# Kernel tuning notes

Measured on AMD Instinct MI355X. Metric: run time of the kernel, lower is better.

## Reference

```python
import jax, jax.numpy as jnp
import numpy as np

B, S, D, H = 4, 1024, 1024, 16
DK = D // H
EPS_LN = 1e-6

def setup_inputs() -> dict:
    key = jax.random.key(0)
    ks = jax.random.split(key, 16)
    sc = 1.0 / np.sqrt(D)
    inp = {}
    names = ['q_r','q_i','k_r','k_i','v_r','v_i']
    for i, n in enumerate(names):
        inp[n] = jax.random.normal(ks[i], (B, S, D), dtype=jnp.float32)
    wnames = ['wq_r','wq_i','wk_r','wk_i','wv_r','wv_i','wfc_r','wfc_i']
    for i, n in enumerate(wnames):
        inp[n] = jax.random.normal(ks[6 + i], (D, D), dtype=jnp.float32) * sc
    inp['gamma'] = jnp.ones((D,), dtype=jnp.float32)
    inp['beta'] = jnp.zeros((D,), dtype=jnp.float32)
    return inp

def _clinear(xr, xi, wr, wi):
    # complex (xr + i*xi) @ (wr + i*wi)^T, weights stored [out, in]
    r = xr @ wr.T - xi @ wi.T
    im = xi @ wr.T + xr @ wi.T
    return r, im

def _forward(q_r, q_i, k_r, k_i, v_r, v_i, wq_r, wq_i, wk_r, wk_i,
             wv_r, wv_i, wfc_r, wfc_i, gamma, beta):
    res_r, res_i = q_r, q_i
    qr, qi = _clinear(q_r, q_i, wq_r, wq_i)
    kr, ki = _clinear(k_r, k_i, wk_r, wk_i)
    vr, vi = _clinear(v_r, v_i, wv_r, wv_i)
    # [B,S,D] -> [B,H,S,DK]
    split = lambda x: x.reshape(B, S, H, DK).transpose(0, 2, 1, 3)
    qr, qi, kr, ki, vr, vi = map(split, (qr, qi, kr, ki, vr, vi))
    temp = jnp.asarray(DK ** 0.5, qr.dtype)
    qr = qr / temp
    qi = qi / temp
    # q @ conj(k)^T : real = qr.kr + qi.ki ; imag = qi.kr - qr.ki
    ar = jnp.einsum('bhqd,bhkd->bhqk', qr, kr) + jnp.einsum('bhqd,bhkd->bhqk', qi, ki)
    ai = jnp.einsum('bhqd,bhkd->bhqk', qi, kr) - jnp.einsum('bhqd,bhkd->bhqk', qr, ki)
    attn = jax.nn.softmax(jnp.sqrt(ar * ar + ai * ai), axis=-1)  # magnitude softmax
    or_ = jnp.einsum('bhqk,bhkd->bhqd', attn, vr)
    oi_ = jnp.einsum('bhqk,bhkd->bhqd', attn, vi)
    merge = lambda x: x.transpose(0, 2, 1, 3).reshape(B, S, D)
    or_, oi_ = merge(or_), merge(oi_)
    fr, fi = _clinear(or_, oi_, wfc_r, wfc_i)
    # ComplexDropout in eval mode: identity except imag += 1e-10
    fi = fi + 1e-10
    xr = fr + res_r
    xi = fi + res_i
    # ComplexLayerNorm: mean over all non-batch dims, elementwise magnitude norm
    mr = jnp.mean(xr, axis=(1, 2), keepdims=True)
    mi = jnp.mean(xi, axis=(1, 2), keepdims=True)
    cr = xr - mr
    ci = xi - mi
    std = jnp.sqrt(cr * cr + ci * ci + EPS_LN)
    yr = gamma * (cr / std) + beta
    yi = gamma * (ci / std)
    return yr, yi, attn

def reference(q_r, q_i, k_r, k_i, v_r, v_i, wq_r, wq_i, wk_r, wk_i,
              wv_r, wv_i, wfc_r, wfc_i, gamma, beta):
    return _forward(q_r, q_i, k_r, k_i, v_r, v_i, wq_r, wq_i, wk_r, wk_i,
                    wv_r, wv_i, wfc_r, wfc_i, gamma, beta)
```

## Files before the change

### kernel.cpp

```cpp
#include <hip/hip_runtime.h>
#include <math.h>

#define NB 4
#define SEQ 1024
#define DIM 1024
#define NH 16
#define DHEAD 64
#define BUFN 4194304ULL
#define WHN  1048576ULL
#define LOG2E 1.4426950408889634f

typedef _Float16 f16x8 __attribute__((ext_vector_type(8)));
typedef _Float16 f16x4 __attribute__((ext_vector_type(4)));
typedef float    f32x4 __attribute__((ext_vector_type(4)));

#define MFMA16 __builtin_amdgcn_mfma_f32_16x16x32_f16

__device__ __forceinline__ void split4(const float4 v, f16x4& h, f16x4& l)
{
    const _Float16 h0=(_Float16)v.x, h1=(_Float16)v.y, h2=(_Float16)v.z, h3=(_Float16)v.w;
    h = (f16x4){h0, h1, h2, h3};
    l = (f16x4){(_Float16)((v.x-(float)h0)*2048.0f),
                (_Float16)((v.y-(float)h1)*2048.0f),
                (_Float16)((v.z-(float)h2)*2048.0f),
                (_Float16)((v.w-(float)h3)*2048.0f)};
}

__global__ __launch_bounds__(256)
void splitx_kernel(const float* __restrict__ xr, const float* __restrict__ xi,
                   _Float16* __restrict__ XS)
{
    const float* x = blockIdx.y ? xi : xr;
    _Float16* h = XS + (size_t)blockIdx.y * 2 * BUFN;
    _Float16* l = h + BUFN;
    const int i = (blockIdx.x * 256 + threadIdx.x) << 2;
    const float4 v = *(const float4*)(x + i);
    f16x4 hh, ll; split4(v, hh, ll);
    *(f16x4*)(h + i) = hh;
    *(f16x4*)(l + i) = ll;
}

__global__ __launch_bounds__(256)
void splitw_kernel(const float* w0, const float* w1, const float* w2, const float* w3,
                   const float* w4, const float* w5, const float* w6, const float* w7,
                   _Float16* __restrict__ WS)
{
    const int y = blockIdx.y;
    const float* x = (y==0)?w0:(y==1)?w1:(y==2)?w2:(y==3)?w3:(y==4)?w4:(y==5)?w5:(y==6)?w6:w7;
    _Float16* h = WS + (size_t)y * 2 * WHN;
    _Float16* l = h + WHN;
    const int i = (blockIdx.x * 256 + threadIdx.x) << 2;
    float4 v = *(const float4*)(x + i);
    v.x *= 64.0f; v.y *= 64.0f; v.z *= 64.0f; v.w *= 64.0f;
    f16x4 hh, ll; split4(v, hh, ll);
    *(f16x4*)(h + i) = hh;
    *(f16x4*)(l + i) = ll;
}

template<int MODE>
__global__ __launch_bounds__(256, 1)
void cgemm16_kernel(const _Float16* __restrict__ Ahr, const _Float16* __restrict__ Alr,
                    const _Float16* __restrict__ Ahi, const _Float16* __restrict__ Ali,
                    const _Float16* __restrict__ Bhr, const _Float16* __restrict__ Blr,
                    const _Float16* __restrict__ Bhi, const _Float16* __restrict__ Bli,
                    float* __restrict__ outr, float* __restrict__ outi,
                    const float* __restrict__ resr, const float* __restrict__ resi,
                    float* __restrict__ msum, float scale)
{
    __shared__ __align__(16) _Float16 As[4][64][40];
    __shared__ __align__(16) _Float16 Bs[4][64][40];
    const int t    = threadIdx.x;
    const int lane = t & 63;
    const int w    = t >> 6;
    const int wm   = w >> 1, wn = w & 1;
    const int lr   = lane & 15;
    const int kc   = (lane >> 4) << 3;
    const int m0   = blockIdx.x * 64;
    const int o0   = blockIdx.y * 64;
    const int srow = t >> 2;
    const int sc8  = (t & 3) << 3;

    const size_t aoff = (size_t)(m0 + srow) * DIM + sc8;
    const size_t boff = (size_t)(o0 + srow) * DIM + sc8;

    f32x4 acc[2][2][4];
    #pragma unroll
    for (int i = 0; i < 2; ++i)
        #pragma unroll
        for (int j = 0; j < 2; ++j)
            #pragma unroll
            for (int c = 0; c < 4; ++c)
                acc[i][j][c] = (f32x4){0.f, 0.f, 0.f, 0.f};

    for (int k0 = 0; k0 < DIM; k0 += 32) {
        const uint4 va0 = *(const uint4*)(Ahr + aoff + k0);
        const uint4 va1 = *(const uint4*)(Alr + aoff + k0);
        const uint4 va2 = *(const uint4*)(Ahi + aoff + k0);
        const uint4 va3 = *(const uint4*)(Ali + aoff + k0);
        const uint4 vb0 = *(const uint4*)(Bhr + boff + k0);
        const uint4 vb1 = *(const uint4*)(Blr + boff + k0);
        const uint4 vb2 = *(const uint4*)(Bhi + boff + k0);
        const uint4 vb3 = *(const uint4*)(Bli + boff + k0);
        __syncthreads();
        *(uint4*)&As[0][srow][sc8] = va0;
        *(uint4*)&As[1][srow][sc8] = va1;
        *(uint4*)&As[2][srow][sc8] = va2;
        *(uint4*)&As[3][srow][sc8] = va3;
        *(uint4*)&Bs[0][srow][sc8] = vb0;
        *(uint4*)&Bs[1][srow][sc8] = vb1;
        *(uint4*)&Bs[2][srow][sc8] = vb2;
        *(uint4*)&Bs[3][srow][sc8] = vb3;
        __syncthreads();

        f16x8 a0[2], a1[2], a2[2], a3[2];
        #pragma unroll
        for (int mt = 0; mt < 2; ++mt) {
            const int ar = wm * 32 + mt * 16 + lr;
            a0[mt] = *(const f16x8*)&As[0][ar][kc];
            a1[mt] = *(const f16x8*)&As[1][ar][kc];
            a2[mt] = *(const f16x8*)&As[2][ar][kc];
            a3[mt] = *(const f16x8*)&As[3][ar][kc];
        }
        #pragma unroll
        for (int nt = 0; nt < 2; ++nt) {
            const int br = wn * 32 + nt * 16 + lr;
            const f16x8 bhr = *(const f16x8*)&Bs[0][br][kc];
            const f16x8 blr = *(const f16x8*)&Bs[1][br][kc];
            const f16x8 bhi = *(const f16x8*)&Bs[2][br][kc];
            const f16x8 bli = *(const f16x8*)&Bs[3][br][kc];
            const f16x8 bhiN = -bhi;
            const f16x8 bliN = -bli;
            #pragma unroll
            for (int mt = 0; mt < 2; ++mt) {
                acc[mt][nt][0] = MFMA16(a0[mt], bhr,  acc[mt][nt][0], 0, 0, 0);
                acc[mt][nt][0] = MFMA16(a2[mt], bhiN, acc[mt][nt][0], 0, 0, 0);
                acc[mt][nt][1] = MFMA16(a0[mt], blr,  acc[mt][nt][1], 0, 0, 0);
                acc[mt][nt][1] = MFMA16(a1[mt], bhr,  acc[mt][nt][1], 0, 0, 0);
                acc[mt][nt][1] = MFMA16(a2[mt], bliN, acc[mt][nt][1], 0, 0, 0);
                acc[mt][nt][1] = MFMA16(a3[mt], bhiN, acc[mt][nt][1], 0, 0, 0);
                acc[mt][nt][2] = MFMA16(a2[mt], bhr,  acc[mt][nt][2], 0, 0, 0);
                acc[mt][nt][2] = MFMA16(a0[mt], bhi,  acc[mt][nt][2], 0, 0, 0);
                acc[mt][nt][3] = MFMA16(a2[mt], blr,  acc[mt][nt][3], 0, 0, 0);
                acc[mt][nt][3] = MFMA16(a3[mt], bhr,  acc[mt][nt][3], 0, 0, 0);
                acc[mt][nt][3] = MFMA16(a0[mt], bli,  acc[mt][nt][3], 0, 0, 0);
                acc[mt][nt][3] = MFMA16(a1[mt], bhi,  acc[mt][nt][3], 0, 0, 0);
            }
        }
    }

    const float INVL = 1.0f / 2048.0f;
    if (MODE == 0) {
        #pragma unroll
        for (int mt = 0; mt < 2; ++mt)
            #pragma unroll
            for (int nt = 0; nt < 2; ++nt)
                #pragma unroll
                for (int r = 0; r < 4; ++r) {
                    const int mrow = m0 + wm * 32 + mt * 16 + ((lane >> 4)) * 4 + r;
                    const int ncol = o0 + wn * 32 + nt * 16 + lr;
                    const float cr = (acc[mt][nt][0][r] + acc[mt][nt][1][r] * INVL) * scale;
                    const float ci = (acc[mt][nt][2][r] + acc[mt][nt][3][r] * INVL) * scale;
                    const int b = mrow >> 10, s = mrow & 1023, h = ncol >> 6, dk = ncol & 63;
                    const size_t idx = (((size_t)b * NH + h) * SEQ + s) * DHEAD + dk;
                    outr[idx] = cr;
                    outi[idx] = ci;
                }
    } else {
        float sr = 0.f, si = 0.f;
        #pragma unroll
        for (int mt = 0; mt < 2; ++mt)
            #pragma unroll
            for (int nt = 0; nt < 2; ++nt)
                #pragma unroll
                for (int r = 0; r < 4; ++r) {
                    const int mrow = m0 + wm * 32 + mt * 16 + ((lane >> 4)) * 4 + r;
                    const int ncol = o0 + wn * 32 + nt * 16 + lr;
                    const size_t idx = (size_t)mrow * DIM + ncol;
                    const float cr = (acc[mt][nt][0][r] + acc[mt][nt][1][r] * INVL) * scale
                                     + resr[idx];
                    const float ci = (acc[mt][nt][2][r] + acc[mt][nt][3][r] * INVL) * scale
                                     + 1e-10f + resi[idx];
                    outr[idx] = cr;
                    outi[idx] = ci;
                    sr += cr; si += ci;
                }
        #pragma unroll
        for (int off = 32; off > 0; off >>= 1) { sr += __shfl_xor(sr, off); si += __shfl_xor(si, off); }
        __shared__ float wsum[8];
        if ((t & 63) == 0) { wsum[w * 2 + 0] = sr; wsum[w * 2 + 1] = si; }
        __syncthreads();
        if (t == 0) {
            atomicAdd(&msum[2 * (m0 >> 10) + 0], wsum[0] + wsum[2] + wsum[4] + wsum[6]);
            atomicAdd(&msum[2 * (m0 >> 10) + 1], wsum[1] + wsum[3] + wsum[5] + wsum[7]);
        }
    }
}

__global__ __launch_bounds__(256)
void vtrans_kernel(const float* __restrict__ VR, const float* __restrict__ VI,
                   _Float16* __restrict__ Trh, _Float16* __restrict__ Trl,
                   _Float16* __restrict__ Tih, _Float16* __restrict__ Til)
{
    __shared__ float sr[64][68];
    __shared__ float si[64][68];
    const int t = threadIdx.x;
    const int kb = blockIdx.x, bh = blockIdx.y;
    const size_t ibase = (size_t)bh * SEQ * DHEAD + (size_t)kb * 64 * DHEAD;
    const int row = t >> 4, c0 = (t & 15) << 2;
    #pragma unroll
    for (int it = 0; it < 4; ++it) {
        const float4 a = *(const float4*)(VR + ibase + (size_t)(row + 16*it) * DHEAD + c0);
        const float4 b = *(const float4*)(VI + ibase + (size_t)(row + 16*it) * DHEAD + c0);
        *(float4*)&sr[row + 16*it][c0] = a;
        *(float4*)&si[row + 16*it][c0] = b;
    }
    __syncthreads();
    const int dk = t >> 2, k0 = (t & 3) << 4;
    f16x8 hr[2], lr8[2], hi8[2], li8[2];
    #pragma unroll
    for (int kk = 0; kk < 16; ++kk) {
        const float xr = sr[k0 + kk][dk];
        const float xi = si[k0 + kk][dk];
        const _Float16 hxr = (_Float16)xr;
        const _Float16 hxi = (_Float16)xi;
        hr[kk>>3][kk&7]  = hxr;
        lr8[kk>>3][kk&7] = (_Float16)((xr - (float)hxr) * 2048.0f);
        hi8[kk>>3][kk&7] = hxi;
        li8[kk>>3][kk&7] = (_Float16)((xi - (float)hxi) * 2048.0f);
    }
    const size_t ob = ((size_t)bh * 64 + dk) * SEQ + kb * 64 + k0;
    *(f16x8*)(Trh + ob) = hr[0];  *(f16x8*)(Trh + ob + 8) = hr[1];
    *(f16x8*)(Trl + ob) = lr8[0]; *(f16x8*)(Trl + ob + 8) = lr8[1];
    *(f16x8*)(Tih + ob) = hi8[0]; *(f16x8*)(Tih + ob + 8) = hi8[1];
    *(f16x8*)(Til + ob) = li8[0]; *(f16x8*)(Til + ob + 8) = li8[1];
}

__global__ __launch_bounds__(256, 1)
void attn_scores_kernel(const float* __restrict__ QR, const float* __restrict__ QI,
                        const float* __restrict__ KR, const float* __restrict__ KI,
                        float* __restrict__ attn, float* __restrict__ Lbuf)
{
    __shared__ __align__(16) _Float16 Ks[4][64][72];
    __shared__ float red[2][64];
    const int t = threadIdx.x;
    const int lane = t & 63;
    const int w = t >> 6, wm = w >> 1, wn = w & 1;
    const int lr = lane & 15, g = lane >> 4, kc = g << 3;
    const int q0 = blockIdx.x * 64;
    const int bh = blockIdx.y;
    const size_t base = (size_t)bh * SEQ * DHEAD;
    const int srow = t >> 2, sc0 = (t & 3) << 4;

    #pragma unroll
    for (int c = 0; c < 4; ++c) {
        const float4 a = *(const float4*)(QR + base + (size_t)(q0 + srow) * DHEAD + sc0 + 4*c);
        const float4 b = *(const float4*)(QI + base + (size_t)(q0 + srow) * DHEAD + sc0 + 4*c);
        f16x4 h, l;
        split4(a, h, l);
        *(f16x4*)&Ks[0][srow][sc0 + 4*c] = h;
        *(f16x4*)&Ks[1][srow][sc0 + 4*c] = l;
        split4(b, h, l);
        *(f16x4*)&Ks[2][srow][sc0 + 4*c] = h;
        *(f16x4*)&Ks[3][srow][sc0 + 4*c] = l;
    }
    __syncthreads();
    f16x8 qhr[2][2], qlr[2][2], qhi[2][2], qli[2][2];
    #pragma unroll
    for (int mt = 0; mt < 2; ++mt) {
        const int row = wm * 32 + mt * 16 + lr;
        #pragma unroll
        for (int ks = 0; ks < 2; ++ks) {
            const int col = ks * 32 + kc;
            qhr[mt][ks] = *(const f16x8*)&Ks[0][row][col];
            qlr[mt][ks] = *(const f16x8*)&Ks[1][row][col];
            qhi[mt][ks] = *(const f16x8*)&Ks[2][row][col];
            qli[mt][ks] = *(const f16x8*)&Ks[3][row][col];
        }
    }

    float lsum[2][4] = {};
    float4 pr[4], pi4[4];
    #pragma unroll
    for (int c = 0; c < 4; ++c) {
        pr[c]  = *(const float4*)(KR + base + (size_t)srow * DHEAD + sc0 + 4*c);
        pi4[c] = *(const float4*)(KI + base + (size_t)srow * DHEAD + sc0 + 4*c);
    }

    for (int kt = 0; kt < 16; ++kt) {
        __syncthreads();
        #pragma unroll
        for (int c = 0; c < 4; ++c) {
            f16x4 h, l;
            split4(pr[c], h, l);
            *(f16x4*)&Ks[0][srow][sc0 + 4*c] = h;
            *(f16x4*)&Ks[1][srow][sc0 + 4*c] = l;
            split4(pi4[c], h, l);
            *(f16x4*)&Ks[2][srow][sc0 + 4*c] = h;
            *(f16x4*)&Ks[3][srow][sc0 + 4*c] = l;
        }
        __syncthreads();
        if (kt < 15) {
            const size_t koff = base + (size_t)((kt + 1) * 64 + srow) * DHEAD;
            #pragma unroll
            for (int c = 0; c < 4; ++c) {
                pr[c]  = *(const float4*)(KR + koff + sc0 + 4*c);
                pi4[c] = *(const float4*)(KI + koff + sc0 + 4*c);
            }
        }
        f32x4 arh[2][2], arl[2][2], aih[2][2], ail[2][2];
        #pragma unroll
        for (int i = 0; i < 2; ++i)
            #pragma unroll
            for (int j = 0; j < 2; ++j) {
                arh[i][j] = (f32x4){0,0,0,0}; arl[i][j] = (f32x4){0,0,0,0};
                aih[i][j] = (f32x4){0,0,0,0}; ail[i][j] = (f32x4){0,0,0,0};
            }
        #pragma unroll
        for (int nt = 0; nt < 2; ++nt) {
            const int brow = wn * 32 + nt * 16 + lr;
            #pragma unroll
            for (int ks = 0; ks < 2; ++ks) {
                const int col = ks * 32 + kc;
                const f16x8 khr = *(const f16x8*)&Ks[0][brow][col];
                const f16x8 klr = *(const f16x8*)&Ks[1][brow][col];
                const f16x8 khi = *(const f16x8*)&Ks[2][brow][col];
                const f16x8 kli = *(const f16x8*)&Ks[3][brow][col];
                const f16x8 khiN = -khi;
                const f16x8 kliN = -kli;
                #pragma unroll
                for (int mt = 0; mt < 2; ++mt) {
                    arh[mt][nt] = MFMA16(qhr[mt][ks], khr,  arh[mt][nt], 0,0,0);
                    arh[mt][nt] = MFMA16(qhi[mt][ks], khi,  arh[mt][nt], 0,0,0);
                    arl[mt][nt] = MFMA16(qhr[mt][ks], klr,  arl[mt][nt], 0,0,0);
                    arl[mt][nt] = MFMA16(qlr[mt][ks], khr,  arl[mt][nt], 0,0,0);
                    arl[mt][nt] = MFMA16(qhi[mt][ks], kli,  arl[mt][nt], 0,0,0);
                    arl[mt][nt] = MFMA16(qli[mt][ks], khi,  arl[mt][nt], 0,0,0);
                    aih[mt][nt] = MFMA16(qhi[mt][ks], khr,  aih[mt][nt], 0,0,0);
                    aih[mt][nt] = MFMA16(qhr[mt][ks], khiN, aih[mt][nt], 0,0,0);
                    ail[mt][nt] = MFMA16(qhi[mt][ks], klr,  ail[mt][nt], 0,0,0);
                    ail[mt][nt] = MFMA16(qli[mt][ks], khr,  ail[mt][nt], 0,0,0);
                    ail[mt][nt] = MFMA16(qhr[mt][ks], kliN, ail[mt][nt], 0,0,0);
                    ail[mt][nt] = MFMA16(qlr[mt][ks], khiN, ail[mt][nt], 0,0,0);
                }
            }
        }
        const float INV = 1.0f / 2048.0f;
        #pragma unroll
        for (int mt = 0; mt < 2; ++mt)
            #pragma unroll
            for (int nt = 0; nt < 2; ++nt)
                #pragma unroll
                for (int r = 0; r < 4; ++r) {
                    const float ar = arh[mt][nt][r] + arl[mt][nt][r] * INV;
                    const float ai = aih[mt][nt][r] + ail[mt][nt][r] * INV;
                    const float s  = sqrtf(ar * ar + ai * ai);
                    const int q = q0 + wm * 32 + mt * 16 + g * 4 + r;
                    const int k = kt * 64 + wn * 32 + nt * 16 + lr;
                    attn[((size_t)bh * SEQ + q) * SEQ + k] = s;
                    lsum[mt][r] += exp2f(s * LOG2E);
                }
    }
    #pragma unroll
    for (int mt = 0; mt < 2; ++mt)
        #pragma unroll
        for (int r = 0; r < 4; ++r) {
            float v = lsum[mt][r];
            v += __shfl_xor(v, 1); v += __shfl_xor(v, 2);
            v += __shfl_xor(v, 4); v += __shfl_xor(v, 8);
            lsum[mt][r] = v;
        }
    if (lr == 0) {
        #pragma unroll
        for (int mt = 0; mt < 2; ++mt)
            #pragma unroll
            for (int r = 0; r < 4; ++r)
                red[wn][wm * 32 + mt * 16 + g * 4 + r] = lsum[mt][r];
    }
    __syncthreads();
    if (t < 64) Lbuf[(size_t)bh * SEQ + q0 + t] = red[0][t] + red[1][t];
}

__global__ __launch_bounds__(256, 1)
void attn_pv_kernel(float* __restrict__ attn, const float* __restrict__ Lbuf,
                    const _Float16* __restrict__ Trh, const _Float16* __restrict__ Trl,
                    const _Float16* __restrict__ Tih, const _Float16* __restrict__ Til,
                    _Float16* __restrict__ XOhr, _Float16* __restrict__ XOlr,
                    _Float16* __restrict__ XOhi, _Float16* __restrict__ XOli)
{
    __shared__ __align__(16) _Float16 Ps[2][64][72];
    __shared__ float invL[64];
    const int t = threadIdx.x;
    const int lane = t & 63;
    const int w = t >> 6, wm = w >> 1, wn = w & 1;
    const int lr = lane & 15, g = lane >> 4, kc = g << 3;
    const int q0 = blockIdx.x * 64;
    const int bh = blockIdx.y;
    const size_t abase = ((size_t)bh * SEQ + q0) * SEQ;
    const size_t vbase = (size_t)bh * 64 * SEQ;

    if (t < 64) invL[t] = 1.0f / Lbuf[(size_t)bh * SEQ + q0 + t];

    const size_t vrow[2] = { vbase + (size_t)(wn * 32 + lr) * SEQ + kc,
                             vbase + (size_t)(wn * 32 + 16 + lr) * SEQ + kc };

    f32x4 orh[2][2], orl[2][2], oih[2][2], oil[2][2];
    #pragma unroll
    for (int i = 0; i < 2; ++i)
        #pragma unroll
        for (int j = 0; j < 2; ++j) {
            orh[i][j] = (f32x4){0,0,0,0}; orl[i][j] = (f32x4){0,0,0,0};
            oih[i][j] = (f32x4){0,0,0,0}; oil[i][j] = (f32x4){0,0,0,0};
        }

    const int prow = t >> 4, pcol = (t & 15) << 2;
    float4 sc[4];
    #pragma unroll
    for (int it = 0; it < 4; ++it)
        sc[it] = *(const float4*)(attn + abase + (size_t)(prow + 16*it) * SEQ + pcol);

    for (int kt = 0; kt < 16; ++kt) {
        __syncthreads();
        #pragma unroll
        for (int it = 0; it < 4; ++it) {
            const int row = prow + 16*it;
            const float inv = invL[row];
            float4 p;
            p.x = exp2f(sc[it].x * LOG2E) * inv;
            p.y = exp2f(sc[it].y * LOG2E) * inv;
            p.z = exp2f(sc[it].z * LOG2E) * inv;
            p.w = exp2f(sc[it].w * LOG2E) * inv;
            *(float4*)(attn + abase + (size_t)row * SEQ + kt * 64 + pcol) = p;
            float4 ps;
            ps.x = p.x * 1024.0f; ps.y = p.y * 1024.0f;
            ps.z = p.z * 1024.0f; ps.w = p.w * 1024.0f;
            f16x4 h, l; split4(ps, h, l);
            *(f16x4*)&Ps[0][row][pcol] = h;
            *(f16x4*)&Ps[1][row][pcol] = l;
        }
        __syncthreads();
        if (kt < 15) {
            #pragma unroll
            for (int it = 0; it < 4; ++it)
                sc[it] = *(const float4*)(attn + abase + (size_t)(prow + 16*it) * SEQ
                                          + (kt + 1) * 64 + pcol);
        }
        #pragma unroll
        for (int ks = 0; ks < 2; ++ks) {
            const int col = ks * 32 + kc;
            f16x8 ph[2], pl[2];
            #pragma unroll
            for (int mt = 0; mt < 2; ++mt) {
                const int row = wm * 32 + mt * 16 + lr;
                ph[mt] = *(const f16x8*)&Ps[0][row][col];
                pl[mt] = *(const f16x8*)&Ps[1][row][col];
            }
            const size_t vcol = (size_t)(kt * 64 + ks * 32);
            #pragma unroll
            for (int nt = 0; nt < 2; ++nt) {
                const size_t vr = vrow[nt] + vcol;
                const f16x8 vhr = *(const f16x8*)(Trh + vr);
                const f16x8 vlr = *(const f16x8*)(Trl + vr);
                const f16x8 vhi = *(const f16x8*)(Tih + vr);
                const f16x8 vli = *(const f16x8*)(Til + vr);
                #pragma unroll
                for (int mt = 0; mt < 2; ++mt) {
                    orh[mt][nt] = MFMA16(ph[mt], vhr, orh[mt][nt], 0,0,0);
                    orl[mt][nt] = MFMA16(ph[mt], vlr, orl[mt][nt], 0,0,0);
                    orl[mt][nt] = MFMA16(pl[mt], vhr, orl[mt][nt], 0,0,0);
                    oih[mt][nt] = MFMA16(ph[mt], vhi, oih[mt][nt], 0,0,0);
                    oil[mt][nt] = MFMA16(ph[mt], vli, oil[mt][nt], 0,0,0);
                    oil[mt][nt] = MFMA16(pl[mt], vhi, oil[mt][nt], 0,0,0);
                }
            }
        }
    }
    const float IL = 1.0f / 2048.0f, SP = 1.0f / 1024.0f;
    const int b = bh >> 4, h = bh & 15;
    #pragma unroll
    for (int mt = 0; mt < 2; ++mt)
        #pragma unroll
        for (int nt = 0; nt < 2; ++nt)
            #pragma unroll
            for (int r = 0; r < 4; ++r) {
                const float orv = (orh[mt][nt][r] + orl[mt][nt][r] * IL) * SP;
                const float oiv = (oih[mt][nt][r] + oil[mt][nt][r] * IL) * SP;
                const int q  = q0 + wm * 32 + mt * 16 + g * 4 + r;
                const int dk = wn * 32 + nt * 16 + lr;
                const size_t addr = ((size_t)b * SEQ + q) * DIM + h * DHEAD + dk;
                _Float16 hh = (_Float16)orv;
                XOhr[addr] = hh;
                XOlr[addr] = (_Float16)((orv - (float)hh) * 2048.0f);
                hh = (_Float16)oiv;
                XOhi[addr] = hh;
                XOli[addr] = (_Float16)((oiv - (float)hh) * 2048.0f);
            }
}

__global__ __launch_bounds__(256)
void ln_kernel(const float* __restrict__ xr, const float* __restrict__ xi,
               const float* __restrict__ msum, const float* __restrict__ gamma,
               const float* __restrict__ beta,
               float* __restrict__ yr, float* __restrict__ yi)
{
    const int gid = blockIdx.x * 256 + threadIdx.x;
    const int flat = gid << 2;
    const int b = flat >> 20;
    const int d = flat & (DIM - 1);
    const float mr = msum[2*b+0] * (1.0f/1048576.0f);
    const float mi = msum[2*b+1] * (1.0f/1048576.0f);
    const float4 vr = *(const float4*)(xr + flat);
    const float4 vi = *(const float4*)(xi + flat);
    const float4 g  = *(const float4*)(gamma + d);
    const float4 bt = *(const float4*)(beta + d);
    float4 or4, oi4;
    {
        float cr = vr.x - mr, ci = vi.x - mi;
        float inv = 1.0f / sqrtf(cr*cr + ci*ci + 1e-6f);
        or4.x = g.x * (cr * inv) + bt.x; oi4.x = g.x * (ci * inv);
    }
    {
        float cr = vr.y - mr, ci = vi.y - mi;
        float inv = 1.0f / sqrtf(cr*cr + ci*ci + 1e-6f);
        or4.y = g.y * (cr * inv) + bt.y; oi4.y = g.y * (ci * inv);
    }
    {
        float cr = vr.z - mr, ci = vi.z - mi;
        float inv = 1.0f / sqrtf(cr*cr + ci*ci + 1e-6f);
        or4.z = g.z * (cr * inv) + bt.z; oi4.z = g.z * (ci * inv);
    }
    {
        float cr = vr.w - mr, ci = vi.w - mi;
        float inv = 1.0f / sqrtf(cr*cr + ci*ci + 1e-6f);
        or4.w = g.w * (cr * inv) + bt.w; oi4.w = g.w * (ci * inv);
    }
    *(float4*)(yr + flat) = or4;
    *(float4*)(yi + flat) = oi4;
}

extern "C" void kernel_launch(void* const* d_in, const int* in_sizes, int n_in,
                              void* d_out, int out_size, void* d_ws, size_t ws_size,
                              hipStream_t stream)
{
    const float* q_r   = (const float*)d_in[0];
    const float* q_i   = (const float*)d_in[1];
    const float* k_r   = (const float*)d_in[2];
    const float* k_i   = (const float*)d_in[3];
    const float* v_r   = (const float*)d_in[4];
    const float* v_i   = (const float*)d_in[5];
    const float* wq_r  = (const float*)d_in[6];
    const float* wq_i  = (const float*)d_in[7];
    const float* wk_r  = (const float*)d_in[8];
    const float* wk_i  = (const float*)d_in[9];
    const float* wv_r  = (const float*)d_in[10];
    const float* wv_i  = (const float*)d_in[11];
    const float* wfc_r = (const float*)d_in[12];
    const float* wfc_i = (const float*)d_in[13];
    const float* gamma = (const float*)d_in[14];
    const float* beta  = (const float*)d_in[15];

    float* ws = (float*)d_ws;
    const size_t BUF = BUFN;
    float* QR   = ws + 0*BUF;
    float* QI   = ws + 1*BUF;
    float* KR   = ws + 2*BUF;
    float* KI   = ws + 3*BUF;
    float* VR   = ws + 4*BUF;
    float* VI   = ws + 5*BUF;
    float* MSUM = ws + 6*BUF;
    float* LBUF = ws + 6*BUF + 16;
    _Float16* F  = (_Float16*)(ws + 6*BUF + 16 + 65536);
    _Float16* XS = F;
    _Float16* VT = F + 4*BUF;
    _Float16* WSp = F + 8*BUF;
    float* XR = QR;
    float* XI = QI;

    float* yr   = (float*)d_out;
    float* yi   = yr + BUF;
    float* attn = yr + 2*BUF;

    const dim3 blk(256);
    const dim3 g_gemm(64, 16);
    const float IWS = 1.0f / 64.0f;

    splitw_kernel<<<dim3(1024, 8), blk, 0, stream>>>(wq_r, wq_i, wk_r, wk_i,
                                                     wv_r, wv_i, wfc_r, wfc_i, WSp);

    splitx_kernel<<<dim3(4096, 2), blk, 0, stream>>>(q_r, q_i, XS);
    cgemm16_kernel<0><<<g_gemm, blk, 0, stream>>>(
        XS + 0*BUF, XS + 1*BUF, XS + 2*BUF, XS + 3*BUF,
        WSp + 0*WHN, WSp + 1*WHN, WSp + 2*WHN, WSp + 3*WHN,
        QR, QI, nullptr, nullptr, nullptr, 0.125f * IWS);

    splitx_kernel<<<dim3(4096, 2), blk, 0, stream>>>(k_r, k_i, XS);
    cgemm16_kernel<0><<<g_gemm, blk, 0, stream>>>(
        XS + 0*BUF, XS + 1*BUF, XS + 2*BUF, XS + 3*BUF,
        WSp + 4*WHN, WSp + 5*WHN, WSp + 6*WHN, WSp + 7*WHN,
        KR, KI, nullptr, nullptr, nullptr, IWS);

    splitx_kernel<<<dim3(4096, 2), blk, 0, stream>>>(v_r, v_i, XS);
    cgemm16_kernel<0><<<g_gemm, blk, 0, stream>>>(
        XS + 0*BUF, XS + 1*BUF, XS + 2*BUF, XS + 3*BUF,
        WSp + 8*WHN, WSp + 9*WHN, WSp + 10*WHN, WSp + 11*WHN,
        VR, VI, nullptr, nullptr, nullptr, IWS);

    vtrans_kernel<<<dim3(16, 64), blk, 0, stream>>>(VR, VI,
        VT + 0*BUF, VT + 1*BUF, VT + 2*BUF, VT + 3*BUF);

    attn_scores_kernel<<<dim3(16, 64), blk, 0, stream>>>(QR, QI, KR, KI, attn, LBUF);

    attn_pv_kernel<<<dim3(16, 64), blk, 0, stream>>>(attn, LBUF,
        VT + 0*BUF, VT + 1*BUF, VT + 2*BUF, VT + 3*BUF,
        XS + 0*BUF, XS + 1*BUF, XS + 2*BUF, XS + 3*BUF);

    hipMemsetAsync(MSUM, 0, 8 * sizeof(float), stream);
    cgemm16_kernel<1><<<g_gemm, blk, 0, stream>>>(
        XS + 0*BUF, XS + 1*BUF, XS + 2*BUF, XS + 3*BUF,
        WSp + 12*WHN, WSp + 13*WHN, WSp + 14*WHN, WSp + 15*WHN,
        XR, XI, q_r, q_i, MSUM, IWS);
    ln_kernel<<<dim3(4096), blk, 0, stream>>>(XR, XI, MSUM, gamma, beta, yr, yi);
}
```

Before: 1.001 ms.

## Emit pre-split fp16 Q/K from projection GEMM and halve PV tile rows

Q and K projection GEMMs gain a new epilogue mode that writes hi/lo fp16 split arrays directly in head-major layout. The attention scores kernel can then copy them straight into shared memory instead of loading fp32 and splitting for every query tile and for every K tile. Separately, the PV kernel now uses 32 query rows per block instead of 64, doubling the grid and reducing per-thread accumulators, presumably to improve occupancy. The cost is that each block re-reads V for fewer rows, so V traffic doubles, and the workspace layout is rearranged.

New measurement: 1.259 ms. 25.8% more time.

```diff
diff --git a/kernel.cpp b/kernel.cpp
--- a/kernel.cpp
+++ b/kernel.cpp
@@ -65,7 +65,9 @@
                     const _Float16* __restrict__ Bhi, const _Float16* __restrict__ Bli,
                     float* __restrict__ outr, float* __restrict__ outi,
                     const float* __restrict__ resr, const float* __restrict__ resi,
-                    float* __restrict__ msum, float scale)
+                    float* __restrict__ msum, float scale,
+                    _Float16* __restrict__ f16hr, _Float16* __restrict__ f16lr,
+                    _Float16* __restrict__ f16hi, _Float16* __restrict__ f16li)
 {
     __shared__ __align__(16) _Float16 As[4][64][40];
     __shared__ __align__(16) _Float16 Bs[4][64][40];
@@ -165,6 +167,26 @@
                     outr[idx] = cr;
                     outi[idx] = ci;
                 }
+    } else if (MODE == 2) {
+        #pragma unroll
+        for (int mt = 0; mt < 2; ++mt)
+            #pragma unroll
+            for (int nt = 0; nt < 2; ++nt)
+                #pragma unroll
+                for (int r = 0; r < 4; ++r) {
+                    const int mrow = m0 + wm * 32 + mt * 16 + ((lane >> 4)) * 4 + r;
+                    const int ncol = o0 + wn * 32 + nt * 16 + lr;
+                    const float cr = (acc[mt][nt][0][r] + acc[mt][nt][1][r] * INVL) * scale;
+                    const float ci = (acc[mt][nt][2][r] + acc[mt][nt][3][r] * INVL) * scale;
+                    const int b = mrow >> 10, s = mrow & 1023, h = ncol >> 6, dk = ncol & 63;
+                    const size_t idx = (((size_t)b * NH + h) * SEQ + s) * DHEAD + dk;
+                    _Float16 hh = (_Float16)cr;
+                    f16hr[idx] = hh;
+                    f16lr[idx] = (_Float16)((cr - (float)hh) * 2048.0f);
+                    hh = (_Float16)ci;
+                    f16hi[idx] = hh;
+                    f16li[idx] = (_Float16)((ci - (float)hh) * 2048.0f);
+                }
     } else {
         float sr = 0.f, si = 0.f;
         #pragma unroll
@@ -236,8 +258,7 @@
 }
 
 __global__ __launch_bounds__(256, 1)
-void attn_scores_kernel(const float* __restrict__ QR, const float* __restrict__ QI,
-                        const float* __restrict__ KR, const float* __restrict__ KI,
+void attn_scores_kernel(const _Float16* __restrict__ QS, const _Float16* __restrict__ KS,
                         float* __restrict__ attn, float* __restrict__ Lbuf)
 {
     __shared__ __align__(16) _Float16 Ks[4][64][72];
@@ -252,16 +273,10 @@
     const int srow = t >> 2, sc0 = (t & 3) << 4;
 
     #pragma unroll
-    for (int c = 0; c < 4; ++c) {
-        const float4 a = *(const float4*)(QR + base + (size_t)(q0 + srow) * DHEAD + sc0 + 4*c);
-        const float4 b = *(const float4*)(QI + base + (size_t)(q0 + srow) * DHEAD + sc0 + 4*c);
-        f16x4 h, l;
-        split4(a, h, l);
-        *(f16x4*)&Ks[0][srow][sc0 + 4*c] = h;
-        *(f16x4*)&Ks[1][srow][sc0 + 4*c] = l;
-        split4(b, h, l);
-        *(f16x4*)&Ks[2][srow][sc0 + 4*c] = h;
-        *(f16x4*)&Ks[3][srow][sc0 + 4*c] = l;
+    for (int arr = 0; arr < 4; ++arr) {
+        const _Float16* src = QS + arr * BUFN + base + (size_t)(q0 + srow) * DHEAD;
+        *(uint4*)&Ks[arr][srow][sc0]     = *(const uint4*)(src + sc0);
+        *(uint4*)&Ks[arr][srow][sc0 + 8] = *(const uint4*)(src + sc0 + 8);
     }
     __syncthreads();
     f16x8 qhr[2][2], qlr[2][2], qhi[2][2], qli[2][2];
@@ -279,32 +294,29 @@
     }
 
     float lsum[2][4] = {};
-    float4 pr[4], pi4[4];
-    #pragma unroll
-    for (int c = 0; c < 4; ++c) {
-        pr[c]  = *(const float4*)(KR + base + (size_t)srow * DHEAD + sc0 + 4*c);
-        pi4[c] = *(const float4*)(KI + base + (size_t)srow * DHEAD + sc0 + 4*c);
+    uint4 pf[4][2];
+    #pragma unroll
+    for (int arr = 0; arr < 4; ++arr) {
+        const _Float16* src = KS + arr * BUFN + base + (size_t)srow * DHEAD;
+        pf[arr][0] = *(const uint4*)(src + sc0);
+        pf[arr][1] = *(const uint4*)(src + sc0 + 8);
     }
 
     for (int kt = 0; kt < 16; ++kt) {
         __syncthreads();
         #pragma unroll
-        for (int c = 0; c < 4; ++c) {
-            f16x4 h, l;
-            split4(pr[c], h, l);
-            *(f16x4*)&Ks[0][srow][sc0 + 4*c] = h;
-            *(f16x4*)&Ks[1][srow][sc0 + 4*c] = l;
-            split4(pi4[c], h, l);
-            *(f16x4*)&Ks[2][srow][sc0 + 4*c] = h;
-            *(f16x4*)&Ks[3][srow][sc0 + 4*c] = l;
+        for (int arr = 0; arr < 4; ++arr) {
+            *(uint4*)&Ks[arr][srow][sc0]     = pf[arr][0];
+            *(uint4*)&Ks[arr][srow][sc0 + 8] = pf[arr][1];
         }
         __syncthreads();
         if (kt < 15) {
             const size_t koff = base + (size_t)((kt + 1) * 64 + srow) * DHEAD;
             #pragma unroll
-            for (int c = 0; c < 4; ++c) {
-                pr[c]  = *(const float4*)(KR + koff + sc0 + 4*c);
-                pi4[c] = *(const float4*)(KI + koff + sc0 + 4*c);
+            for (int arr = 0; arr < 4; ++arr) {
+                const _Float16* src = KS + arr * BUFN + koff;
+                pf[arr][0] = *(const uint4*)(src + sc0);
+                pf[arr][1] = *(const uint4*)(src + sc0 + 8);
             }
         }
         f32x4 arh[2][2], arl[2][2], aih[2][2], ail[2][2];
@@ -387,41 +399,40 @@
                     _Float16* __restrict__ XOhr, _Float16* __restrict__ XOlr,
                     _Float16* __restrict__ XOhi, _Float16* __restrict__ XOli)
 {
-    __shared__ __align__(16) _Float16 Ps[2][64][72];
-    __shared__ float invL[64];
+    __shared__ __align__(16) _Float16 Psh[32][72];
+    __shared__ __align__(16) _Float16 Psl[32][72];
+    __shared__ float invL[32];
     const int t = threadIdx.x;
     const int lane = t & 63;
     const int w = t >> 6, wm = w >> 1, wn = w & 1;
     const int lr = lane & 15, g = lane >> 4, kc = g << 3;
-    const int q0 = blockIdx.x * 64;
+    const int q0 = blockIdx.x * 32;
     const int bh = blockIdx.y;
     const size_t abase = ((size_t)bh * SEQ + q0) * SEQ;
     const size_t vbase = (size_t)bh * 64 * SEQ;
 
-    if (t < 64) invL[t] = 1.0f / Lbuf[(size_t)bh * SEQ + q0 + t];
-
-    const size_t vrow[2] = { vbase + (size_t)(wn * 32 + lr) * SEQ + kc,
+    if (t < 32) invL[t] = 1.0f / Lbuf[(size_t)bh * SEQ + q0 + t];
+
+    const size_t voff[2] = { vbase + (size_t)(wn * 32 + lr) * SEQ + kc,
                              vbase + (size_t)(wn * 32 + 16 + lr) * SEQ + kc };
 
-    f32x4 orh[2][2], orl[2][2], oih[2][2], oil[2][2];
-    #pragma unroll
-    for (int i = 0; i < 2; ++i)
-        #pragma unroll
-        for (int j = 0; j < 2; ++j) {
-            orh[i][j] = (f32x4){0,0,0,0}; orl[i][j] = (f32x4){0,0,0,0};
-            oih[i][j] = (f32x4){0,0,0,0}; oil[i][j] = (f32x4){0,0,0,0};
-        }
+    f32x4 orh[2], orl[2], oih[2], oil[2];
+    #pragma unroll
+    for (int nt = 0; nt < 2; ++nt) {
+        orh[nt] = (f32x4){0,0,0,0}; orl[nt] = (f32x4){0,0,0,0};
+        oih[nt] = (f32x4){0,0,0,0}; oil[nt] = (f32x4){0,0,0,0};
+    }
 
     const int prow = t >> 4, pcol = (t & 15) << 2;
-    float4 sc[4];
-    #pragma unroll
-    for (int it = 0; it < 4; ++it)
+    float4 sc[2];
+    #pragma unroll
+    for (int it = 0; it < 2; ++it)
         sc[it] = *(const float4*)(attn + abase + (size_t)(prow + 16*it) * SEQ + pcol);
 
     for (int kt = 0; kt < 16; ++kt) {
         __syncthreads();
         #pragma unroll
-        for (int it = 0; it < 4; ++it) {
+        for (int it = 0; it < 2; ++it) {
             const int row = prow + 16*it;
             const float inv = invL[row];
             float4 p;
@@ -434,66 +445,57 @@
             ps.x = p.x * 1024.0f; ps.y = p.y * 1024.0f;
             ps.z = p.z * 1024.0f; ps.w = p.w * 1024.0f;
             f16x4 h, l; split4(ps, h, l);
-            *(f16x4*)&Ps[0][row][pcol] = h;
-            *(f16x4*)&Ps[1][row][pcol] = l;
+            *(f16x4*)&Psh[row][pcol] = h;
+            *(f16x4*)&Psl[row][pcol] = l;
         }
         __syncthreads();
         if (kt < 15) {
             #pragma unroll
-            for (int it = 0; it < 4; ++it)
+            for (int it = 0; it < 2; ++it)
                 sc[it] = *(const float4*)(attn + abase + (size_t)(prow + 16*it) * SEQ
                                           + (kt + 1) * 64 + pcol);
         }
         #pragma unroll
         for (int ks = 0; ks < 2; ++ks) {
             const int col = ks * 32 + kc;
-            f16x8 ph[2], pl[2];
-            #pragma unroll
-            for (int mt = 0; mt < 2; ++mt) {
-                const int row = wm * 32 + mt * 16 + lr;
-                ph[mt] = *(const f16x8*)&Ps[0][row][col];
-                pl[mt] = *(const f16x8*)&Ps[1][row][col];
-            }
+            const int row = wm * 16 + lr;
+            const f16x8 ph = *(const f16x8*)&Psh[row][col];
+            const f16x8 pl = *(const f16x8*)&Psl[row][col];
             const size_t vcol = (size_t)(kt * 64 + ks * 32);
             #pragma unroll
             for (int nt = 0; nt < 2; ++nt) {
-                const size_t vr = vrow[nt] + vcol;
-                const f16x8 vhr = *(const f16x8*)(Trh + vr);
-                const f16x8 vlr = *(const f16x8*)(Trl + vr);
-                const f16x8 vhi = *(const f16x8*)(Tih + vr);
-                const f16x8 vli = *(const f16x8*)(Til + vr);
-                #pragma unroll
-                for (int mt = 0; mt < 2; ++mt) {
-                    orh[mt][nt] = MFMA16(ph[mt], vhr, orh[mt][nt], 0,0,0);
-                    orl[mt][nt] = MFMA16(ph[mt], vlr, orl[mt][nt], 0,0,0);
-                    orl[mt][nt] = MFMA16(pl[mt], vhr, orl[mt][nt], 0,0,0);
-                    oih[mt][nt] = MFMA16(ph[mt], vhi, oih[mt][nt], 0,0,0);
-                    oil[mt][nt] = MFMA16(ph[mt], vli, oil[mt][nt], 0,0,0);
-                    oil[mt][nt] = MFMA16(pl[mt], vhi, oil[mt][nt], 0,0,0);
-                }
+                const size_t vo = voff[nt] + vcol;
+                const f16x8 vhr = *(const f16x8*)(Trh + vo);
+                const f16x8 vlr = *(const f16x8*)(Trl + vo);
+                const f16x8 vhi = *(const f16x8*)(Tih + vo);
+                const f16x8 vli = *(const f16x8*)(Til + vo);
+                orh[nt] = MFMA16(ph, vhr, orh[nt], 0,0,0);
+                orl[nt] = MFMA16(ph, vlr, orl[nt], 0,0,0);
+                orl[nt] = MFMA16(pl, vhr, orl[nt], 0,0,0);
+                oih[nt] = MFMA16(ph, vhi, oih[nt], 0,0,0);
+                oil[nt] = MFMA16(ph, vli, oil[nt], 0,0,0);
+                oil[nt] = MFMA16(pl, vhi, oil[nt], 0,0,0);
             }
         }
     }
     const float IL = 1.0f / 2048.0f, SP = 1.0f / 1024.0f;
     const int b = bh >> 4, h = bh & 15;
     #pragma unroll
-    for (int mt = 0; mt < 2; ++mt)
-        #pragma unroll
-        for (int nt = 0; nt < 2; ++nt)
-            #pragma unroll
-            for (int r = 0; r < 4; ++r) {
-                const float orv = (orh[mt][nt][r] + orl[mt][nt][r] * IL) * SP;
-                const float oiv = (oih[mt][nt][r] + oil[mt][nt][r] * IL) * SP;
-                const int q  = q0 + wm * 32 + mt * 16 + g * 4 + r;
-                const int dk = wn * 32 + nt * 16 + lr;
-                const size_t addr = ((size_t)b * SEQ + q) * DIM + h * DHEAD + dk;
-                _Float16 hh = (_Float16)orv;
-                XOhr[addr] = hh;
-                XOlr[addr] = (_Float16)((orv - (float)hh) * 2048.0f);
-                hh = (_Float16)oiv;
-                XOhi[addr] = hh;
-                XOli[addr] = (_Float16)((oiv - (float)hh) * 2048.0f);
-            }
+    for (int nt = 0; nt < 2; ++nt)
+        #pragma unroll
+        for (int r = 0; r < 4; ++r) {
+            const float orv = (orh[nt][r] + orl[nt][r] * IL) * SP;
+            const float oiv = (oih[nt][r] + oil[nt][r] * IL) * SP;
+            const int q  = q0 + wm * 16 + g * 4 + r;
+            const int dk = wn * 32 + nt * 16 + lr;
+            const size_t addr = ((size_t)b * SEQ + q) * DIM + h * DHEAD + dk;
+            _Float16 hh = (_Float16)orv;
+            XOhr[addr] = hh;
+            XOlr[addr] = (_Float16)((orv - (float)hh) * 2048.0f);
+            hh = (_Float16)oiv;
+            XOhi[addr] = hh;
+            XOli[addr] = (_Float16)((oiv - (float)hh) * 2048.0f);
+        }
 }
 
 __global__ __launch_bounds__(256)
@@ -560,20 +562,18 @@
 
     float* ws = (float*)d_ws;
     const size_t BUF = BUFN;
-    float* QR   = ws + 0*BUF;
-    float* QI   = ws + 1*BUF;
-    float* KR   = ws + 2*BUF;
-    float* KI   = ws + 3*BUF;
-    float* VR   = ws + 4*BUF;
-    float* VI   = ws + 5*BUF;
-    float* MSUM = ws + 6*BUF;
-    float* LBUF = ws + 6*BUF + 16;
-    _Float16* F  = (_Float16*)(ws + 6*BUF + 16 + 65536);
+    float* VR   = ws + 0*BUF;
+    float* VI   = ws + 1*BUF;
+    float* XR   = ws + 2*BUF;
+    float* XI   = ws + 3*BUF;
+    float* MSUM = ws + 4*BUF;
+    float* LBUF = ws + 4*BUF + 16;
+    _Float16* F  = (_Float16*)(ws + 4*BUF + 16 + 65536);
     _Float16* XS = F;
     _Float16* VT = F + 4*BUF;
-    _Float16* WSp = F + 8*BUF;
-    float* XR = QR;
-    float* XI = QI;
+    _Float16* QS = F + 8*BUF;
+    _Float16* KS = F + 12*BUF;
+    _Float16* WSp = F + 16*BUF;
 
     float* yr   = (float*)d_out;
     float* yi   = yr + BUF;
@@ -587,29 +587,32 @@
                                                      wv_r, wv_i, wfc_r, wfc_i, WSp);
 
     splitx_kernel<<<dim3(4096, 2), blk, 0, stream>>>(q_r, q_i, XS);
-    cgemm16_kernel<0><<<g_gemm, blk, 0, stream>>>(
+    cgemm16_kernel<2><<<g_gemm, blk, 0, stream>>>(
         XS + 0*BUF, XS + 1*BUF, XS + 2*BUF, XS + 3*BUF,
         WSp + 0*WHN, WSp + 1*WHN, WSp + 2*WHN, WSp + 3*WHN,
-        QR, QI, nullptr, nullptr, nullptr, 0.125f * IWS);
+        nullptr, nullptr, nullptr, nullptr, nullptr, 0.125f * IWS,
+        QS + 0*BUF, QS + 1*BUF, QS + 2*BUF, QS + 3*BUF);
 
     splitx_kernel<<<dim3(4096, 2), blk, 0, stream>>>(k_r, k_i, XS);
-    cgemm16_kernel<0><<<g_gemm, blk, 0, stream>>>(
+    cgemm16_kernel<2><<<g_gemm, blk, 0, stream>>>(
         XS + 0*BUF, XS + 1*BUF, XS + 2*BUF, XS + 3*BUF,
         WSp + 4*WHN, WSp + 5*WHN, WSp + 6*WHN, WSp + 7*WHN,
-        KR, KI, nullptr, nullptr, nullptr, IWS);
+        nullptr, nullptr, nullptr, nullptr, nullptr, IWS,
+        KS + 0*BUF, KS + 1*BUF, KS + 2*BUF, KS + 3*BUF);
 
     splitx_kernel<<<dim3(4096, 2), blk, 0, stream>>>(v_r, v_i, XS);
     cgemm16_kernel<0><<<g_gemm, blk, 0, stream>>>(
         XS + 0*BUF, XS + 1*BUF, XS + 2*BUF, XS + 3*BUF,
         WSp + 8*WHN, WSp + 9*WHN, WSp + 10*WHN, WSp + 11*WHN,
-        VR, VI, nullptr, nullptr, nullptr, IWS);
+        VR, VI, nullptr, nullptr, nullptr, IWS,
+        nullptr, nullptr, nullptr, nullptr);
 
     vtrans_kernel<<<dim3(16, 64), blk, 0, stream>>>(VR, VI,
         VT + 0*BUF, VT + 1*BUF, VT + 2*BUF, VT + 3*BUF);
 
-    attn_scores_kernel<<<dim3(16, 64), blk, 0, stream>>>(QR, QI, KR, KI, attn, LBUF);
-
-    attn_pv_kernel<<<dim3(16, 64), blk, 0, stream>>>(attn, LBUF,
+    attn_scores_kernel<<<dim3(16, 64), blk, 0, stream>>>(QS, KS, attn, LBUF);
+
+    attn_pv_kernel<<<dim3(32, 64), blk, 0, stream>>>(attn, LBUF,
         VT + 0*BUF, VT + 1*BUF, VT + 2*BUF, VT + 3*BUF,
         XS + 0*BUF, XS + 1*BUF, XS + 2*BUF, XS + 3*BUF);
 
@@ -617,6 +620,7 @@
     cgemm16_kernel<1><<<g_gemm, blk, 0, stream>>>(
         XS + 0*BUF, XS + 1*BUF, XS + 2*BUF, XS + 3*BUF,
         WSp + 12*WHN, WSp + 13*WHN, WSp + 14*WHN, WSp + 15*WHN,
-        XR, XI, q_r, q_i, MSUM, IWS);
+        XR, XI, q_r, q_i, MSUM, IWS,
+        nullptr, nullptr, nullptr, nullptr);
     ln_kernel<<<dim3(4096), blk, 0, stream>>>(XR, XI, MSUM, gamma, beta, yr, yi);
 }
```
